# Optimization experiments

Measured on AMD Instinct MI355X. Metric: run time of the kernel, lower is better.

The kernel has to match this reference:

```python
import jax, jax.numpy as jnp
import numpy as np

B, N, DIM, H, DH = 8, 1024, 1024, 16, 64

def setup_inputs() -> dict:
    key = jax.random.key(0)
    ks = jax.random.split(key, 6)
    return {
        'x': jax.random.normal(ks[0], (B, N, DIM), dtype=jnp.float32),
        'freqs': jax.random.normal(ks[1], (1, N, DH), dtype=jnp.float32),
        'bias': jax.random.normal(ks[2], (1, N, DH), dtype=jnp.float32),
        'ln_gamma': jnp.ones((DIM,), jnp.float32),
        'ln_beta': jnp.zeros((DIM,), jnp.float32),
        'w_qk': jax.random.normal(ks[3], (DIM, 2 * H * DH), dtype=jnp.float32) * (DIM ** -0.5),
        'w_v': jax.random.normal(ks[4], (DIM, H * DH), dtype=jnp.float32) * (DIM ** -0.5),
        'w_out': jax.random.normal(ks[5], (H * DH, DIM), dtype=jnp.float32) * ((H * DH) ** -0.5),
        'b_out': jnp.zeros((DIM,), jnp.float32),
    }

def _apply_polar(t, freqs):
    # t: [b,h,n,d]; freqs: [1,n,d] broadcast over b,h. Output doubles last dim.
    t = jax.nn.softplus(t)
    return jnp.concatenate((t * jnp.cos(freqs), t * jnp.sin(freqs)), axis=-1)

def reference(x, freqs, bias, ln_gamma, ln_beta, w_qk, w_v, w_out, b_out):
    eps = 1e-5
    mu = jnp.mean(x, axis=-1, keepdims=True)
    var = jnp.var(x, axis=-1, keepdims=True)
    xn = (x - mu) * jax.lax.rsqrt(var + eps) * ln_gamma + ln_beta
    qk = jnp.einsum('bnd,de->bne', xn, w_qk)
    q, k = jnp.split(qk, 2, axis=-1)
    v = jnp.einsum('bnd,de->bne', xn, w_v)
    split_heads = lambda t: t.reshape(B, N, H, DH).transpose(0, 2, 1, 3)
    q, k, v = split_heads(q), split_heads(k), split_heads(v)
    q = _apply_polar(q, freqs)          # [b,h,n,2*DH]
    k = _apply_polar(k, freqs + bias)   # [b,h,n,2*DH]
    scale = DH ** -0.5
    dots = jnp.einsum('bhnd,bhmd->bhnm', q, k) * scale
    attn = jax.nn.softmax(dots, axis=-1)
    out = jnp.einsum('bhnm,bhmd->bhnd', attn, v)
    out = out.transpose(0, 2, 1, 3).reshape(B, N, H * DH)
    return jnp.einsum('bne,ed->bnd', out, w_out) + b_out
```

## Files before the change

kernel.cpp:

```cpp
#include <hip/hip_runtime.h>
#include <cmath>

using f16   = _Float16;
using f16x2 = __attribute__((ext_vector_type(2))) _Float16;
using f16x4 = __attribute__((ext_vector_type(4))) _Float16;
using f16x8 = __attribute__((ext_vector_type(8))) _Float16;
using f32x4 = __attribute__((ext_vector_type(4))) float;

#define DEV __device__ __forceinline__

constexpr int Bb  = 8;
constexpr int Nn  = 1024;
constexpr int DIM = 1024;
constexpr int Hh  = 16;
constexpr int DH  = 64;
constexpr int EQKV = 3072;

DEV void async16(const f16* g, f16* l) {
  __builtin_amdgcn_global_load_lds(
      (const __attribute__((address_space(1))) void*)g,
      (__attribute__((address_space(3))) void*)l, 16, 0, 0);
}

DEV float softplusf(float x) {
  return fmaxf(x, 0.f) + __logf(1.f + __expf(-fabsf(x)));
}

__global__ __launch_bounds__(256) void prep_kernel(const float* __restrict__ s0,
                                                   const float* __restrict__ s1,
                                                   const float* __restrict__ s2,
                                                   f16* __restrict__ d0,
                                                   f16* __restrict__ d2,
                                                   const float* __restrict__ freqs,
                                                   const float* __restrict__ fbias,
                                                   float2* __restrict__ trigQ,
                                                   float2* __restrict__ trigK,
                                                   const float* __restrict__ x,
                                                   const float* __restrict__ gamma,
                                                   const float* __restrict__ beta,
                                                   f16* __restrict__ xn) {
  __shared__ float tile[32][33];
  __shared__ float red[8];
  int bz = blockIdx.z;
  int t = threadIdx.x;

  if (bz < 3) {
    const float* src; f16* dst; int cols;
    if (bz == 0)      { src = s0; dst = d0;                        cols = 2048; }
    else if (bz == 1) { src = s1; dst = d0 + (size_t)2048 * 1024;  cols = 1024; }
    else              { src = s2; dst = d2;                        cols = 1024; }
    int c0 = blockIdx.x * 32, r0 = blockIdx.y * 32;
    if (c0 >= cols) return;
    int tx = t & 31, ty = t >> 5;
#pragma unroll
    for (int j = 0; j < 32; j += 8)
      tile[ty + j][tx] = src[(size_t)(r0 + ty + j) * cols + c0 + tx];
    __syncthreads();
#pragma unroll
    for (int j = 0; j < 32; j += 8)
      dst[(size_t)(c0 + ty + j) * 1024 + r0 + tx] = (f16)tile[tx][ty + j];
  } else if (bz == 3) {
    int blk = blockIdx.y * 64 + blockIdx.x;
    if (blk >= 256) return;
    int i = blk * 256 + t;
    float f = freqs[i], fb = fbias[i];
    float cq, sq, ck, sk;
    __sincosf(f, &sq, &cq);
    __sincosf(f + fb, &sk, &ck);
    trigQ[i] = make_float2(cq, sq);
    trigK[i] = make_float2(ck, sk);
  } else {
    int row = (bz - 4) * 2048 + blockIdx.y * 64 + blockIdx.x;
    const float4* xr = (const float4*)(x + (size_t)row * DIM);
    float4 v = xr[t];
    float s  = v.x + v.y + v.z + v.w;
    float s2 = v.x * v.x + v.y * v.y + v.z * v.z + v.w * v.w;
#pragma unroll
    for (int off = 32; off; off >>= 1) {
      s  += __shfl_xor(s,  off, 64);
      s2 += __shfl_xor(s2, off, 64);
    }
    int wv = t >> 6, lane = t & 63;
    if (lane == 0) { red[wv] = s; red[4 + wv] = s2; }
    __syncthreads();
    s  = red[0] + red[1] + red[2] + red[3];
    s2 = red[4] + red[5] + red[6] + red[7];
    float mu  = s * (1.f / DIM);
    float var = s2 * (1.f / DIM) - mu * mu;
    float rs  = rsqrtf(var + 1e-5f);
    float4 g = ((const float4*)gamma)[t];
    float4 bb = ((const float4*)beta)[t];
    f16x4 o;
    o[0] = (f16)((v.x - mu) * rs * g.x + bb.x);
    o[1] = (f16)((v.y - mu) * rs * g.y + bb.y);
    o[2] = (f16)((v.z - mu) * rs * g.z + bb.z);
    o[3] = (f16)((v.w - mu) * rs * g.w + bb.w);
    ((f16x4*)(xn + (size_t)row * DIM))[t] = o;
  }
}

template <bool FP32OUT>
__global__ __launch_bounds__(256) void gemm_bt(const f16* __restrict__ A,
                                               const f16* __restrict__ Bt,
                                               void* __restrict__ Cv,
                                               const float* __restrict__ bias,
                                               int M, int K, int E) {
  __shared__ f16 lA[128 * 32];
  __shared__ f16 lB[128 * 32];
  int tid  = threadIdx.x;
  int lane = tid & 63;
  int wv   = __builtin_amdgcn_readfirstlane(tid >> 6);
  int nbe  = E >> 7;
  const int cpx = gridDim.x >> 3;
  int bid = blockIdx.x;
  int swz = (bid & 7) * cpx + (bid >> 3);
  int bm = swz / nbe, be = swz % nbe;
  size_t m0 = (size_t)bm * 128, e0 = (size_t)be * 128;
  int wm = (wv & 1) * 64, we = (wv >> 1) * 64;
  int lm = lane & 15, q = lane >> 4;

  f32x4 acc[4][4] = {};

  int row_s[2], cg_s[2];
#pragma unroll
  for (int r = 0; r < 2; ++r) {
    int s = r * 256 + tid;
    row_s[r] = s >> 2;
    cg_s[r]  = (s & 3) ^ ((row_s[r] >> 1) & 3);
  }
  const f16* pa[4];
  const f16* pb[4];
#pragma unroll
  for (int i = 0; i < 4; ++i) {
    int ra = wm + i * 16 + lm;
    pa[i] = lA + ra * 32 + (q ^ ((ra >> 1) & 3)) * 8;
    int rb = we + i * 16 + lm;
    pb[i] = lB + rb * 32 + (q ^ ((rb >> 1) & 3)) * 8;
  }

  for (int k0 = 0; k0 < K; k0 += 32) {
#pragma unroll
    for (int r = 0; r < 2; ++r) {
      const f16* ga = A  + (m0 + row_s[r]) * K + k0 + cg_s[r] * 8;
      const f16* gb = Bt + (e0 + row_s[r]) * K + k0 + cg_s[r] * 8;
      async16(ga, lA + (r * 256 + wv * 64) * 8);
      async16(gb, lB + (r * 256 + wv * 64) * 8);
    }
    __syncthreads();
    f16x8 af[4], bf[4];
#pragma unroll
    for (int i = 0; i < 4; ++i) {
      af[i] = *(const f16x8*)pa[i];
      bf[i] = *(const f16x8*)pb[i];
    }
#pragma unroll
    for (int i = 0; i < 4; ++i)
#pragma unroll
      for (int j = 0; j < 4; ++j)
        acc[i][j] = __builtin_amdgcn_mfma_f32_16x16x32_f16(af[i], bf[j], acc[i][j], 0, 0, 0);
    __syncthreads();
  }

#pragma unroll
  for (int i = 0; i < 4; ++i) {
    size_t mbase = m0 + wm + i * 16 + q * 4;
#pragma unroll
    for (int j = 0; j < 4; ++j) {
      size_t e = e0 + we + j * 16 + lm;
#pragma unroll
      for (int g = 0; g < 4; ++g) {
        float val = acc[i][j][g];
        if (FP32OUT)
          ((float*)Cv)[(mbase + g) * (size_t)E + e] = val + bias[e];
        else
          ((f16*)Cv)[(mbase + g) * (size_t)E + e] = (f16)val;
      }
    }
  }
}

__global__ __launch_bounds__(256, 4) void gemm_qkv(const f16* __restrict__ A,
                                                   const f16* __restrict__ Bt,
                                                   f16* __restrict__ Qp,
                                                   f16* __restrict__ Kp,
                                                   f16* __restrict__ Vt,
                                                   const float2* __restrict__ trigQ,
                                                   const float2* __restrict__ trigK,
                                                   int M, int K) {
  __shared__ f16 smem[17408];
  f16* lA = smem;
  f16* lB = smem + 4096;
  int tid  = threadIdx.x;
  int lane = tid & 63;
  int wv   = __builtin_amdgcn_readfirstlane(tid >> 6);
  const int nbe = 24;
  const int cpx = gridDim.x >> 3;
  int bid = blockIdx.x;
  int swz = (bid & 7) * cpx + (bid >> 3);
  int bm = swz / nbe, be = swz % nbe;
  size_t m0 = (size_t)bm * 128, e0 = (size_t)be * 128;
  int wm = (wv & 1) * 64, we = (wv >> 1) * 64;
  int lm = lane & 15, q = lane >> 4;

  f32x4 acc[4][4] = {};

  int row_s[2], cg_s[2];
#pragma unroll
  for (int r = 0; r < 2; ++r) {
    int s = r * 256 + tid;
    row_s[r] = s >> 2;
    cg_s[r]  = (s & 3) ^ ((row_s[r] >> 1) & 3);
  }
  const f16* pa[4];
  const f16* pb[4];
#pragma unroll
  for (int i = 0; i < 4; ++i) {
    int ra = wm + i * 16 + lm;
    pa[i] = lA + ra * 32 + (q ^ ((ra >> 1) & 3)) * 8;
    int rb = we + i * 16 + lm;
    pb[i] = lB + rb * 32 + (q ^ ((rb >> 1) & 3)) * 8;
  }

  for (int k0 = 0; k0 < K; k0 += 32) {
#pragma unroll
    for (int r = 0; r < 2; ++r) {
      const f16* ga = A  + (m0 + row_s[r]) * K + k0 + cg_s[r] * 8;
      const f16* gb = Bt + (e0 + row_s[r]) * K + k0 + cg_s[r] * 8;
      async16(ga, lA + (r * 256 + wv * 64) * 8);
      async16(gb, lB + (r * 256 + wv * 64) * 8);
    }
    __syncthreads();
    f16x8 af[4], bf[4];
#pragma unroll
    for (int i = 0; i < 4; ++i) {
      af[i] = *(const f16x8*)pa[i];
      bf[i] = *(const f16x8*)pb[i];
    }
#pragma unroll
    for (int i = 0; i < 4; ++i)
#pragma unroll
      for (int j = 0; j < 4; ++j)
        acc[i][j] = __builtin_amdgcn_mfma_f32_16x16x32_f16(af[i], bf[j], acc[i][j], 0, 0, 0);
    __syncthreads();
  }

  const int sec = be >> 3;
  if (sec < 2) {
    f16* dst = (sec == 0) ? Qp : Kp;
    const float2* trig = (sec == 0) ? trigQ : trigK;
    const float scl = (sec == 0) ? 0.125f : 1.0f;
#pragma unroll
    for (int i = 0; i < 4; ++i) {
      size_t mbase = m0 + wm + i * 16 + q * 4;
#pragma unroll
      for (int j = 0; j < 4; ++j) {
        int hd = (int)((e0 + we + j * 16 + lm) & 1023);
        int h = hd >> 6, d = hd & 63;
#pragma unroll
        for (int g = 0; g < 4; ++g) {
          size_t tok = mbase + g;
          int n = (int)(tok & 1023);
          size_t bh = (tok >> 10) * 16 + h;
          float sp = softplusf(acc[i][j][g]) * scl;
          float2 T = trig[n * 64 + d];
          f16x2 o = { (f16)(sp * T.x), (f16)(sp * T.y) };
          *(f16x2*)(dst + (bh * (size_t)Nn + n) * 128 + 2 * d) = o;
        }
      }
    }
  } else {
    __syncthreads();
#pragma unroll
    for (int i = 0; i < 4; ++i) {
      int nl = wm + i * 16 + q * 4;
#pragma unroll
      for (int j = 0; j < 4; ++j) {
        int ds = we + j * 16 + lm;
#pragma unroll
        for (int g = 0; g < 4; ++g)
          smem[ds * 136 + nl + g] = (f16)acc[i][j][g];
      }
    }
    __syncthreads();
    const int nbase = (int)(m0 & 1023);
    const size_t bh0 = (m0 >> 10) * 16 + ((e0 & 1023) >> 6);
#pragma unroll
    for (int k = 0; k < 8; ++k) {
      int c = k * 256 + tid;
      int row = c >> 4, ch = c & 15;
      int h = row >> 6, d = row & 63;
      f16x8 v8 = *(const f16x8*)(smem + row * 136 + ch * 8);
      *(f16x8*)(Vt + ((bh0 + h) * (size_t)64 + d) * Nn + nbase + ch * 8) = v8;
    }
  }
}

constexpr int VK0 = 0;
constexpr int VK1 = 8192;
constexpr int VV0 = 16384;
constexpr int VV1 = 21504;
constexpr int VEND = 26624;

__global__ __launch_bounds__(256, 3) void attn_kernel(const f16* __restrict__ Qp,
                                                      const f16* __restrict__ Kp,
                                                      const f16* __restrict__ Vt,
                                                      f16* __restrict__ attout) {
  __shared__ f16 smem[VEND];

  int tid = threadIdx.x, lane = tid & 63;
  int wv = __builtin_amdgcn_readfirstlane(tid >> 6);
  int lm = lane & 15, q = lane >> 4;
  int bx = blockIdx.x;
  int bh = (bx & 7) | ((bx >> 6) << 3);
  int qt = (bx >> 3) & 7;
  const f16* Kbase = Kp + (size_t)bh * Nn * 128;
  const f16* Vbase = Vt + (size_t)bh * 64 * Nn;

  {
    int idx = tid * 4;
    f16 val = (idx < 64) ? (f16)1.0f : (f16)0.0f;
    f16x4 v4 = {val, val, val, val};
    *(f16x4*)(smem + VV0 + 64 * 64 + idx) = v4;
    *(f16x4*)(smem + VV1 + 64 * 64 + idx) = v4;
  }

#pragma unroll
  for (int i = 0; i < 4; ++i) {
    int s = i * 256 + tid;
    int r = s >> 4, c = s & 15;
    int g = c ^ (r & 15);
    async16(Kbase + (size_t)r * 128 + g * 8, smem + VK0 + (i * 256 + wv * 64) * 8);
  }
#pragma unroll
  for (int i = 0; i < 2; ++i) {
    int s = i * 256 + tid;
    int r = s >> 3, c = s & 7;
    int g = c ^ (r & 7);
    async16(Vbase + (size_t)r * Nn + g * 8, smem + VV0 + (i * 256 + wv * 64) * 8);
  }

  f16x8 qf[2][4];
  {
    const f16* Qb = Qp + ((size_t)bh * Nn + qt * 128 + wv * 32) * 128;
#pragma unroll
    for (int grp = 0; grp < 2; ++grp)
#pragma unroll
      for (int ks = 0; ks < 4; ++ks)
        qf[grp][ks] = *(const f16x8*)(Qb + (size_t)(grp * 16 + lm) * 128 + ks * 32 + q * 8);
  }

  f32x4 O[2][5] = {};
  float mrow[2] = {-INFINITY, -INFINITY};

  for (int kt = 0; kt < 16; ++kt) {
    __syncthreads();

    if (kt < 15) {
      f16* nK = smem + ((kt & 1) ? VK0 : VK1);
      f16* nV = smem + ((kt & 1) ? VV0 : VV1);
#pragma unroll
      for (int i = 0; i < 4; ++i) {
        int s = i * 256 + tid;
        int r = s >> 4, c = s & 15;
        int g = c ^ (r & 15);
        async16(Kbase + (size_t)((kt + 1) * 64 + r) * 128 + g * 8, nK + (i * 256 + wv * 64) * 8);
      }
#pragma unroll
      for (int i = 0; i < 2; ++i) {
        int s = i * 256 + tid;
        int r = s >> 3, c = s & 7;
        int g = c ^ (r & 7);
        async16(Vbase + (size_t)r * Nn + (kt + 1) * 64 + g * 8, nV + (i * 256 + wv * 64) * 8);
      }
    }
    const f16* sK = smem + ((kt & 1) ? VK1 : VK0);
    const f16* sV = smem + ((kt & 1) ? VV1 : VV0);

    f32x4 S[2][4] = {};
#pragma unroll
    for (int nt = 0; nt < 4; ++nt) {
      f16x8 kf[4];
#pragma unroll
      for (int ks = 0; ks < 4; ++ks)
        kf[ks] = *(const f16x8*)(sK + (nt * 16 + lm) * 128 + (((ks * 4 + q) ^ lm) * 8));
#pragma unroll
      for (int ks = 0; ks < 4; ++ks) {
        S[0][nt] = __builtin_amdgcn_mfma_f32_16x16x32_f16(kf[ks], qf[0][ks], S[0][nt], 0, 0, 0);
        S[1][nt] = __builtin_amdgcn_mfma_f32_16x16x32_f16(kf[ks], qf[1][ks], S[1][nt], 0, 0, 0);
      }
    }

    f16x4 pf[2][4];
#pragma unroll
    for (int grp = 0; grp < 2; ++grp) {
      float mx = -INFINITY;
#pragma unroll
      for (int nt = 0; nt < 4; ++nt)
#pragma unroll
        for (int g = 0; g < 4; ++g) mx = fmaxf(mx, S[grp][nt][g]);
      mx = fmaxf(mx, __shfl_xor(mx, 16, 64));
      mx = fmaxf(mx, __shfl_xor(mx, 32, 64));
      float mn = fmaxf(mrow[grp], mx);
      float alpha = __expf(mrow[grp] - mn);
      mrow[grp] = mn;
#pragma unroll
      for (int nt = 0; nt < 4; ++nt)
#pragma unroll
        for (int g = 0; g < 4; ++g)
          pf[grp][nt][g] = (f16)__expf(S[grp][nt][g] - mn);
#pragma unroll
      for (int nto = 0; nto < 5; ++nto)
#pragma unroll
        for (int g = 0; g < 4; ++g) O[grp][nto][g] *= alpha;
    }

#pragma unroll
    for (int nto = 0; nto < 5; ++nto) {
      int r = nto * 16 + lm;
#pragma unroll
      for (int nt = 0; nt < 4; ++nt) {
        int c16 = (nt * 2 + (q >> 1)) ^ (r & 7);
        f16x4 vf = *(const f16x4*)(sV + r * 64 + c16 * 8 + (q & 1) * 4);
        O[0][nto] = __builtin_amdgcn_mfma_f32_16x16x16f16(vf, pf[0][nt], O[0][nto], 0, 0, 0);
        O[1][nto] = __builtin_amdgcn_mfma_f32_16x16x16f16(vf, pf[1][nt], O[1][nto], 0, 0, 0);
      }
    }
  }

  int b = bh >> 4, h = bh & 15;
#pragma unroll
  for (int grp = 0; grp < 2; ++grp) {
    float l = __shfl(O[grp][4][0], lm, 64);
    float inv = 1.f / l;
    size_t token = (size_t)b * Nn + qt * 128 + wv * 32 + grp * 16 + lm;
#pragma unroll
    for (int nto = 0; nto < 4; ++nto) {
      f16x4 o4;
#pragma unroll
      for (int g = 0; g < 4; ++g) o4[g] = (f16)(O[grp][nto][g] * inv);
      *(f16x4*)(attout + token * (size_t)(Hh * DH) + h * 64 + nto * 16 + q * 4) = o4;
    }
  }
}

extern "C" void kernel_launch(void* const* d_in, const int* in_sizes, int n_in,
                              void* d_out, int out_size, void* d_ws, size_t ws_size,
                              hipStream_t stream) {
  const float* x     = (const float*)d_in[0];
  const float* freqs = (const float*)d_in[1];
  const float* fbias = (const float*)d_in[2];
  const float* gamma = (const float*)d_in[3];
  const float* beta  = (const float*)d_in[4];
  const float* w_qk  = (const float*)d_in[5];
  const float* w_v   = (const float*)d_in[6];
  const float* w_out = (const float*)d_in[7];
  const float* b_out = (const float*)d_in[8];
  float* out = (float*)d_out;

  const size_t T = (size_t)Bb * Nn;
  f16* WqkvT = (f16*)d_ws;
  f16* WoutT = WqkvT + (size_t)EQKV * DIM;
  float2* trigQ = (float2*)(WoutT + (size_t)DIM * DIM);
  float2* trigK = trigQ + (size_t)Nn * DH;
  f16* Xn    = (f16*)(trigK + (size_t)Nn * DH);
  f16* AttO  = Xn + T * DIM;
  f16* Qp    = AttO + T * DIM;
  f16* Kp    = Qp + (size_t)128 * Nn * 128;
  f16* Vt    = Kp + (size_t)128 * Nn * 128;

  prep_kernel<<<dim3(64, 32, 8), 256, 0, stream>>>(
      w_qk, w_v, w_out, WqkvT, WoutT, freqs, fbias, trigQ, trigK,
      x, gamma, beta, Xn);

  gemm_qkv<<<(int)(T / 128) * (EQKV / 128), 256, 0, stream>>>(
      Xn, WqkvT, Qp, Kp, Vt, trigQ, trigK, (int)T, DIM);

  attn_kernel<<<Bb * Hh * (Nn / 128), 256, 0, stream>>>(Qp, Kp, Vt, AttO);

  gemm_bt<true><<<(int)(T / 128) * (DIM / 128), 256, 0, stream>>>(
      AttO, WoutT, (void*)out, b_out, (int)T, DIM, DIM);
}
```

Measured before the change: 274.5 us.

## Drop LDS staging in attention; read K/V fragments directly from global memory

```diff
diff --git a/kernel.cpp b/kernel.cpp
--- a/kernel.cpp
+++ b/kernel.cpp
@@ -295,50 +295,19 @@
   }
 }
 
-constexpr int VK0 = 0;
-constexpr int VK1 = 8192;
-constexpr int VV0 = 16384;
-constexpr int VV1 = 21504;
-constexpr int VEND = 26624;
-
-__global__ __launch_bounds__(256, 3) void attn_kernel(const f16* __restrict__ Qp,
+__global__ __launch_bounds__(256, 4) void attn_kernel(const f16* __restrict__ Qp,
                                                       const f16* __restrict__ Kp,
                                                       const f16* __restrict__ Vt,
                                                       f16* __restrict__ attout) {
-  __shared__ f16 smem[VEND];
-
   int tid = threadIdx.x, lane = tid & 63;
+  int lm = lane & 15, q = lane >> 4;
   int wv = __builtin_amdgcn_readfirstlane(tid >> 6);
-  int lm = lane & 15, q = lane >> 4;
   int bx = blockIdx.x;
   int bh = (bx & 7) | ((bx >> 6) << 3);
   int qt = (bx >> 3) & 7;
   const f16* Kbase = Kp + (size_t)bh * Nn * 128;
   const f16* Vbase = Vt + (size_t)bh * 64 * Nn;
 
-  {
-    int idx = tid * 4;
-    f16 val = (idx < 64) ? (f16)1.0f : (f16)0.0f;
-    f16x4 v4 = {val, val, val, val};
-    *(f16x4*)(smem + VV0 + 64 * 64 + idx) = v4;
-    *(f16x4*)(smem + VV1 + 64 * 64 + idx) = v4;
-  }
-
-#pragma unroll
-  for (int i = 0; i < 4; ++i) {
-    int s = i * 256 + tid;
-    int r = s >> 4, c = s & 15;
-    int g = c ^ (r & 15);
-    async16(Kbase + (size_t)r * 128 + g * 8, smem + VK0 + (i * 256 + wv * 64) * 8);
-  }
-#pragma unroll
-  for (int i = 0; i < 2; ++i) {
-    int s = i * 256 + tid;
-    int r = s >> 3, c = s & 7;
-    int g = c ^ (r & 7);
-    async16(Vbase + (size_t)r * Nn + g * 8, smem + VV0 + (i * 256 + wv * 64) * 8);
-  }
-
   f16x8 qf[2][4];
   {
     const f16* Qb = Qp + ((size_t)bh * Nn + qt * 128 + wv * 32) * 128;
@@ -351,30 +320,12 @@
 
   f32x4 O[2][5] = {};
   float mrow[2] = {-INFINITY, -INFINITY};
+  const f16x4 vones = {(f16)1.f, (f16)1.f, (f16)1.f, (f16)1.f};
+  const f16x4 vzero = {(f16)0.f, (f16)0.f, (f16)0.f, (f16)0.f};
+  const f16x4 vsyn  = (lm == 0) ? vones : vzero;
 
   for (int kt = 0; kt < 16; ++kt) {
-    __syncthreads();
-
-    if (kt < 15) {
-      f16* nK = smem + ((kt & 1) ? VK0 : VK1);
-      f16* nV = smem + ((kt & 1) ? VV0 : VV1);
-#pragma unroll
-      for (int i = 0; i < 4; ++i) {
-        int s = i * 256 + tid;
-        int r = s >> 4, c = s & 15;
-        int g = c ^ (r & 15);
-        async16(Kbase + (size_t)((kt + 1) * 64 + r) * 128 + g * 8, nK + (i * 256 + wv * 64) * 8);
-      }
-#pragma unroll
-      for (int i = 0; i < 2; ++i) {
-        int s = i * 256 + tid;
-        int r = s >> 3, c = s & 7;
-        int g = c ^ (r & 7);
-        async16(Vbase + (size_t)r * Nn + (kt + 1) * 64 + g * 8, nV + (i * 256 + wv * 64) * 8);
-      }
-    }
-    const f16* sK = smem + ((kt & 1) ? VK1 : VK0);
-    const f16* sV = smem + ((kt & 1) ? VV1 : VV0);
+    const f16* Kt = Kbase + (size_t)kt * 64 * 128;
 
     f32x4 S[2][4] = {};
 #pragma unroll
@@ -382,7 +333,7 @@
       f16x8 kf[4];
 #pragma unroll
       for (int ks = 0; ks < 4; ++ks)
-        kf[ks] = *(const f16x8*)(sK + (nt * 16 + lm) * 128 + (((ks * 4 + q) ^ lm) * 8));
+        kf[ks] = *(const f16x8*)(Kt + (size_t)(nt * 16 + lm) * 128 + ks * 32 + q * 8);
 #pragma unroll
       for (int ks = 0; ks < 4; ++ks) {
         S[0][nt] = __builtin_amdgcn_mfma_f32_16x16x32_f16(kf[ks], qf[0][ks], S[0][nt], 0, 0, 0);
@@ -415,15 +366,19 @@
     }
 
 #pragma unroll
-    for (int nto = 0; nto < 5; ++nto) {
-      int r = nto * 16 + lm;
+    for (int nto = 0; nto < 4; ++nto) {
+      const f16* Vr = Vbase + (size_t)(nto * 16 + lm) * Nn + kt * 64;
 #pragma unroll
       for (int nt = 0; nt < 4; ++nt) {
-        int c16 = (nt * 2 + (q >> 1)) ^ (r & 7);
-        f16x4 vf = *(const f16x4*)(sV + r * 64 + c16 * 8 + (q & 1) * 4);
+        f16x4 vf = *(const f16x4*)(Vr + nt * 16 + q * 4);
         O[0][nto] = __builtin_amdgcn_mfma_f32_16x16x16f16(vf, pf[0][nt], O[0][nto], 0, 0, 0);
         O[1][nto] = __builtin_amdgcn_mfma_f32_16x16x16f16(vf, pf[1][nt], O[1][nto], 0, 0, 0);
       }
+    }
+#pragma unroll
+    for (int nt = 0; nt < 4; ++nt) {
+      O[0][4] = __builtin_amdgcn_mfma_f32_16x16x16f16(vsyn, pf[0][nt], O[0][4], 0, 0, 0);
+      O[1][4] = __builtin_amdgcn_mfma_f32_16x16x16f16(vsyn, pf[1][nt], O[1][4], 0, 0, 0);
     }
   }
 
```

Result: slower. 438.1 us (+59.6%).
